# Kernel tuning notes

Measured on AMD Instinct MI355X. Metric: run time of the kernel, lower is better.

## Reference

```python
import jax, jax.numpy as jnp
import numpy as np

D_MODEL = 1024
NUM_HEADS = 16
D_FF = 4096
EPS = 1e-5


def setup_inputs() -> dict:
    key = jax.random.key(0)
    ks = jax.random.split(key, 8)
    B, S, D = 4, 2048, D_MODEL
    s = 1.0 / np.sqrt(D)
    return {
        "x": jax.random.normal(ks[0], (B, S, D), jnp.float32),
        "ln1_w": jnp.ones((D,), jnp.float32),
        "ln2_w": jnp.ones((D,), jnp.float32),
        "wq": jax.random.normal(ks[1], (D, D), jnp.float32) * s,
        "wk": jax.random.normal(ks[2], (D, D), jnp.float32) * s,
        "wv": jax.random.normal(ks[3], (D, D), jnp.float32) * s,
        "wo": jax.random.normal(ks[4], (D, D), jnp.float32) * s,
        "w1": jax.random.normal(ks[5], (D_FF, D), jnp.float32) * s,
        "w2": jax.random.normal(ks[6], (D, D_FF), jnp.float32) * (1.0 / np.sqrt(D_FF)),
    }


def rmsnorm(a, w):
    # (a * w) / sqrt(mean(a^2) + eps)  -- matches torch module exactly
    denom = jnp.sqrt(jnp.mean(jnp.square(a), axis=-1, keepdims=True) + EPS)
    return a * w / denom


def attention(x, wq, wk, wv, wo):
    B, S, D = x.shape
    H, dk = NUM_HEADS, D // NUM_HEADS
    q = (x @ wq.T).reshape(B, S, H, dk).transpose(0, 2, 1, 3)  # B H S dk
    k = (x @ wk.T).reshape(B, S, H, dk).transpose(0, 2, 1, 3)
    v = (x @ wv.T).reshape(B, S, H, dk).transpose(0, 2, 1, 3)
    scores = jnp.einsum("bhqd,bhkd->bhqk", q, k) / np.sqrt(dk)
    causal = jnp.triu(jnp.ones((S, S), bool), k=1)
    scores = jnp.where(causal, -jnp.inf, scores)
    probs = jax.nn.softmax(scores, axis=-1)
    out = jnp.einsum("bhqk,bhkd->bhqd", probs, v)
    out = out.transpose(0, 2, 1, 3).reshape(B, S, D)
    return out @ wo.T


def ffn(x, w1, w2):
    h = x @ w1.T
    h = 0.5 * h * (1.0 + jax.lax.erf(h / np.sqrt(2.0).astype(np.float32)))
    return h @ w2.T


def reference(x, ln1_w, ln2_w, wq, wk, wv, wo, w1, w2):
    y = x + attention(rmsnorm(x, ln1_w), wq, wk, wv, wo)
    return y + ffn(rmsnorm(y, ln2_w), w1, w2)
```

## Files before the change

### kernel.cpp

```cpp
#include <hip/hip_runtime.h>

#define DM    1024
#define DFF   4096
#define SEQ   2048
#define BATCH 4
#define NROWS (BATCH * SEQ)
#define HEADS 16
#define DKH   64
#define KSTR  (2 * DM)

typedef __attribute__((ext_vector_type(4))) float          f32x4;
typedef __attribute__((ext_vector_type(8))) __bf16         bf16x8;
typedef __attribute__((ext_vector_type(8))) unsigned short u16x8;
typedef __attribute__((ext_vector_type(4))) unsigned short u16x4;

static __device__ __forceinline__ unsigned short f2bf(float f) {
  unsigned u = __builtin_bit_cast(unsigned, f);
  u += 0x7fffu + ((u >> 16) & 1u);
  return (unsigned short)(u >> 16);
}

struct CvtJobs {
  const float* src[6];
  unsigned short* dst[6];
};
__constant__ const unsigned c_cum[6] = {262144u, 524288u, 786432u, 1048576u, 2097152u, 3145728u};

__global__ __launch_bounds__(256) void k_f2bf_all(CvtJobs jobs) {
  unsigned i = blockIdx.x * blockDim.x + threadIdx.x;
  if (i >= 3145728u) return;
  int j = 0;
#pragma unroll
  for (int s = 0; s < 6; ++s) j += (i >= c_cum[s]) ? 1 : 0;
  const unsigned base = (j == 0) ? 0u : c_cum[j - 1];
  const unsigned loc  = i - base;
  float4 v = reinterpret_cast<const float4*>(jobs.src[j])[loc];
  ushort4 o;
  o.x = f2bf(v.x); o.y = f2bf(v.y); o.z = f2bf(v.z); o.w = f2bf(v.w);
  reinterpret_cast<ushort4*>(jobs.dst[j])[loc] = o;
}

__global__ __launch_bounds__(256) void k_rmsnorm(const float* __restrict__ x,
                                                 const float* __restrict__ w,
                                                 unsigned short* __restrict__ out) {
  const int row = blockIdx.x;
  const float4 v = reinterpret_cast<const float4*>(x + (size_t)row * DM)[threadIdx.x];
  float ss = v.x * v.x + v.y * v.y + v.z * v.z + v.w * v.w;
#pragma unroll
  for (int off = 32; off > 0; off >>= 1) ss += __shfl_down(ss, off);
  __shared__ float red[4];
  if ((threadIdx.x & 63) == 0) red[threadIdx.x >> 6] = ss;
  __syncthreads();
  const float tot  = red[0] + red[1] + red[2] + red[3];
  const float rden = rsqrtf(tot * (1.0f / DM) + 1e-5f);
  const float4 wv = reinterpret_cast<const float4*>(w)[threadIdx.x];
  ushort4 o;
  o.x = f2bf(v.x * wv.x * rden);
  o.y = f2bf(v.y * wv.y * rden);
  o.z = f2bf(v.z * wv.z * rden);
  o.w = f2bf(v.w * wv.w * rden);
  reinterpret_cast<ushort4*>(out + (size_t)row * DM)[threadIdx.x] = o;
}

template <int EPI, int TN, int BK>
__global__ __launch_bounds__(256, 2) void k_gemm_nt(const unsigned short* __restrict__ A,
                                                    const unsigned short* __restrict__ B,
                                                    void* __restrict__ Cv,
                                                    const float* __restrict__ res,
                                                    int M, int N, int K) {
  constexpr int NW = TN / 128;
  alignas(16) __shared__ unsigned short As[2][128 * BK];
  alignas(16) __shared__ unsigned short Bs[2][128 * NW * BK];
  const int t  = threadIdx.x;
  const int w  = t >> 6;
  const int l  = t & 63;
  const int wr = w >> 1, wc = w & 1;
  const int lr = l & 15, lk = l >> 4;

  const unsigned bid = blockIdx.y * gridDim.x + blockIdx.x;
  const unsigned cpx = (gridDim.x * gridDim.y) >> 3;
  const unsigned sw  = (bid & 7) * cpx + (bid >> 3);
  const int m0 = (int)(sw / gridDim.x) * 128;
  const int n0 = (int)(sw % gridDim.x) * TN;

  auto stage = [&](int buf, int k0) {
    if constexpr (BK == 32) {
      const int srow = t >> 2;
      const int sgr  = (t & 3) ^ (srow & 3);
#pragma unroll
      for (int r = 0; r < 2; ++r) {
        const unsigned short* ga = A + (size_t)(m0 + r * 64 + srow) * K + k0 + 8 * sgr;
        __builtin_amdgcn_global_load_lds((__attribute__((address_space(1))) void*)ga,
                                         (__attribute__((address_space(3))) void*)(&As[buf][r * 2048 + w * 512]),
                                         16, 0, 0);
      }
#pragma unroll
      for (int r = 0; r < 2 * NW; ++r) {
        const unsigned short* gb = B + (size_t)(n0 + r * 64 + srow) * K + k0 + 8 * sgr;
        __builtin_amdgcn_global_load_lds((__attribute__((address_space(1))) void*)gb,
                                         (__attribute__((address_space(3))) void*)(&Bs[buf][r * 2048 + w * 512]),
                                         16, 0, 0);
      }
    } else {
      const int srow8 = l >> 3;
      const int g     = l & 7;
#pragma unroll
      for (int i = 0; i < 4; ++i) {
        const int row = i * 32 + w * 8 + srow8;
        const int sg  = g ^ (row & 7);
        const unsigned short* ga = A + (size_t)(m0 + row) * K + k0 + 8 * sg;
        __builtin_amdgcn_global_load_lds((__attribute__((address_space(1))) void*)ga,
                                         (__attribute__((address_space(3))) void*)(&As[buf][i * 2048 + w * 512]),
                                         16, 0, 0);
        const unsigned short* gb = B + (size_t)(n0 + row) * K + k0 + 8 * sg;
        __builtin_amdgcn_global_load_lds((__attribute__((address_space(1))) void*)gb,
                                         (__attribute__((address_space(3))) void*)(&Bs[buf][i * 2048 + w * 512]),
                                         16, 0, 0);
      }
    }
  };

  f32x4 acc[4][4 * NW] = {};

  stage(0, 0);
  const int nIt = K / BK;
  for (int it = 0; it < nIt; ++it) {
    const int buf = it & 1;
    __syncthreads();
    if (it + 1 < nIt) stage(buf ^ 1, (it + 1) * BK);

    if constexpr (BK == 32) {
      bf16x8 af[4], bf[4 * NW];
#pragma unroll
      for (int m = 0; m < 4; ++m)
        af[m] = *reinterpret_cast<const bf16x8*>(
            &As[buf][(wr * 64 + m * 16 + lr) * 32 + 8 * (lk ^ (lr & 3))]);
#pragma unroll
      for (int n = 0; n < 4 * NW; ++n)
        bf[n] = *reinterpret_cast<const bf16x8*>(
            &Bs[buf][(wc * 64 * NW + n * 16 + lr) * 32 + 8 * (lk ^ (lr & 3))]);
#pragma unroll
      for (int m = 0; m < 4; ++m)
#pragma unroll
        for (int n = 0; n < 4 * NW; ++n)
          acc[m][n] = __builtin_amdgcn_mfma_f32_16x16x32_bf16(af[m], bf[n], acc[m][n], 0, 0, 0);
    } else {
#pragma unroll
      for (int kk = 0; kk < 2; ++kk) {
        bf16x8 af[4], bf[4];
#pragma unroll
        for (int m = 0; m < 4; ++m)
          af[m] = *reinterpret_cast<const bf16x8*>(
              &As[buf][(wr * 64 + m * 16 + lr) * 64 + 8 * ((4 * kk + lk) ^ (lr & 7))]);
#pragma unroll
        for (int n = 0; n < 4; ++n)
          bf[n] = *reinterpret_cast<const bf16x8*>(
              &Bs[buf][(wc * 64 + n * 16 + lr) * 64 + 8 * ((4 * kk + lk) ^ (lr & 7))]);
#pragma unroll
        for (int m = 0; m < 4; ++m)
#pragma unroll
          for (int n = 0; n < 4; ++n)
            acc[m][n] = __builtin_amdgcn_mfma_f32_16x16x32_bf16(af[m], bf[n], acc[m][n], 0, 0, 0);
      }
    }
  }

#pragma unroll
  for (int m = 0; m < 4; ++m) {
#pragma unroll
    for (int n = 0; n < 4 * NW; ++n) {
#pragma unroll
      for (int r = 0; r < 4; ++r) {
        const size_t row = (size_t)(m0 + wr * 64 + m * 16 + lk * 4 + r);
        const size_t col = (size_t)(n0 + wc * 64 * NW + n * 16 + lr);
        const float a = acc[m][n][r];
        if constexpr (EPI == 0) {
          ((unsigned short*)Cv)[row * N + col] = f2bf(a);
        } else if constexpr (EPI == 1) {
          ((float*)Cv)[row * N + col] = a + res[row * N + col];
        } else if constexpr (EPI == 2) {
          const float h2 = a * a;
          const float e  = exp2f(a * (2.30221535f + 0.10295355f * h2));
          const float g  = a - a / (e + 1.0f);
          ((unsigned short*)Cv)[row * N + col] = f2bf(g);
        } else {
          const float sc = (col < DM) ? 0.18033688011f : 1.0f;
          ((unsigned short*)Cv)[row * N + col] = f2bf(a * sc);
        }
      }
    }
  }
}

__global__ __launch_bounds__(256, 3) void k_attn(const unsigned short* __restrict__ QK,
                                                 const unsigned short* __restrict__ VT,
                                                 unsigned short* __restrict__ O) {
  const int h   = blockIdx.x;
  const int qtA = blockIdx.y;
  const int qtB = 31 - qtA;
  const int b   = blockIdx.z;
  const int t  = threadIdx.x, w = t >> 6, l = t & 63;
  const int lr = l & 15, lk = l >> 4;
  const size_t rowB = (size_t)b * SEQ;
  const int hoff  = h * DKH;
  const int qw2[2] = { qtA * 64 + 16 * w, qtB * 64 + 16 * w };

  alignas(16) __shared__ unsigned short Ks[128 * 64];
  alignas(16) __shared__ unsigned short Vt[64 * 128];
  alignas(16) __shared__ unsigned short Ps[2][4][16 * 64];

  char* const KsB = (char*)Ks;
  char* const VtB = (char*)Vt;

  auto stage = [&](int kb2) {
#pragma unroll
    for (int i = 0; i < 4; ++i) {
      const int krow = 32 * w + 8 * i + (l >> 3);
      const int sgk  = (l & 7) ^ (krow & 7);
      const unsigned short* gk = QK + (size_t)(rowB + kb2 + krow) * KSTR + DM + hoff + 8 * sgk;
      __builtin_amdgcn_global_load_lds((__attribute__((address_space(1))) void*)gk,
                                       (__attribute__((address_space(3))) void*)(KsB + w * 4096 + i * 1024),
                                       16, 0, 0);
      const int vrow = 16 * w + 4 * i + (l >> 4);
      const int sgv  = (l & 15) ^ (vrow & 15);
      const unsigned short* gv = VT + (size_t)(hoff + vrow) * NROWS + rowB + kb2 + 8 * sgv;
      __builtin_amdgcn_global_load_lds((__attribute__((address_space(1))) void*)gv,
                                       (__attribute__((address_space(3))) void*)(VtB + w * 4096 + i * 1024),
                                       16, 0, 0);
    }
  };

  bf16x8 qf[2][2];
#pragma unroll
  for (int s = 0; s < 2; ++s)
#pragma unroll
    for (int kk = 0; kk < 2; ++kk)
      qf[s][kk] = *reinterpret_cast<const bf16x8*>(
          QK + (rowB + qw2[s] + lr) * KSTR + hoff + 32 * kk + 8 * lk);

  f32x4 oacc[2][4] = {};
  float mrun[2] = {-1e30f, -1e30f};
  float lrun[2] = {0.0f, 0.0f};

  const int ktmax = qtB >> 1;
  for (int kt = 0; kt <= ktmax; ++kt) {
    const int kbase = kt * 128;
    __syncthreads();
    stage(kbase);
    __syncthreads();

#pragma unroll
    for (int h2 = 0; h2 < 2; ++h2) {
      const int kb = kbase + 64 * h2;
      const bool act[2] = { kb <= qw2[0] + 15, kb <= qw2[1] + 15 };
      if (!act[0] && !act[1]) continue;
      const char* Kc = KsB + h2 * 8192;

      f32x4 sacc[2][4] = {};
      __builtin_amdgcn_s_setprio(1);
#pragma unroll
      for (int tt = 0; tt < 4; ++tt) {
        bf16x8 kf0 = *reinterpret_cast<const bf16x8*>(Kc + (16 * tt + lr) * 128 + 16 * ((lk + 0) ^ (lr & 7)));
        bf16x8 kf1 = *reinterpret_cast<const bf16x8*>(Kc + (16 * tt + lr) * 128 + 16 * ((lk + 4) ^ (lr & 7)));
#pragma unroll
        for (int s = 0; s < 2; ++s) {
          if (!act[s]) continue;
          sacc[s][tt] = __builtin_amdgcn_mfma_f32_16x16x32_bf16(kf0, qf[s][0], sacc[s][tt], 0, 0, 0);
          sacc[s][tt] = __builtin_amdgcn_mfma_f32_16x16x32_bf16(kf1, qf[s][1], sacc[s][tt], 0, 0, 0);
        }
      }
      __builtin_amdgcn_s_setprio(0);

#pragma unroll
      for (int s = 0; s < 2; ++s) {
        if (!act[s]) continue;
        const int qw = qw2[s];
        char* const PsSB = (char*)(Ps[s][w]);
        const int qg = qw + lr;
        float sv[4][4];
        if (kb + 63 > qw) {
#pragma unroll
          for (int tt = 0; tt < 4; ++tt)
#pragma unroll
            for (int r = 0; r < 4; ++r) {
              const int kg = kb + 16 * tt + 4 * lk + r;
              sv[tt][r] = (kg > qg) ? -1e30f : sacc[s][tt][r];
            }
        } else {
#pragma unroll
          for (int tt = 0; tt < 4; ++tt)
#pragma unroll
            for (int r = 0; r < 4; ++r) sv[tt][r] = sacc[s][tt][r];
        }
        const float a0 = fmaxf(fmaxf(sv[0][0], sv[0][1]), sv[0][2]);
        const float a1 = fmaxf(fmaxf(sv[0][3], sv[1][0]), sv[1][1]);
        const float a2 = fmaxf(fmaxf(sv[1][2], sv[1][3]), sv[2][0]);
        const float a3 = fmaxf(fmaxf(sv[2][1], sv[2][2]), sv[2][3]);
        const float a4 = fmaxf(fmaxf(sv[3][0], sv[3][1]), sv[3][2]);
        float tm = fmaxf(fmaxf(fmaxf(a0, a1), a2), fmaxf(fmaxf(a3, a4), sv[3][3]));
        tm = fmaxf(tm, __shfl_xor(tm, 16));
        tm = fmaxf(tm, __shfl_xor(tm, 32));
        float mref = mrun[s];
        if (__any(tm > mref + 8.0f)) {
          const float mnew  = fmaxf(mref, tm);
          const float alpha = exp2f(mref - mnew);
#pragma unroll
          for (int r = 0; r < 4; ++r) {
            const float ar = __shfl(alpha, 4 * lk + r);
#pragma unroll
            for (int dn = 0; dn < 4; ++dn) oacc[s][dn][r] *= ar;
          }
          lrun[s] *= alpha;
          mrun[s] = mnew;
          mref = mnew;
        }
        float p[4][4];
        unsigned short pb[4][4];
#pragma unroll
        for (int tt = 0; tt < 4; ++tt)
#pragma unroll
          for (int r = 0; r < 4; ++r) {
            p[tt][r] = exp2f(sv[tt][r] - mref);
            pb[tt][r] = __builtin_bit_cast(unsigned short, static_cast<__bf16>(p[tt][r]));
          }
        float t0 = (p[0][0] + p[0][1]) + (p[0][2] + p[0][3]);
        float t1 = (p[1][0] + p[1][1]) + (p[1][2] + p[1][3]);
        float t2 = (p[2][0] + p[2][1]) + (p[2][2] + p[2][3]);
        float t3 = (p[3][0] + p[3][1]) + (p[3][2] + p[3][3]);
        float ts = (t0 + t1) + (t2 + t3);
        ts += __shfl_xor(ts, 16);
        ts += __shfl_xor(ts, 32);
        lrun[s] += ts;
#pragma unroll
        for (int tt = 0; tt < 4; ++tt) {
          u16x4 pw = {pb[tt][0], pb[tt][1], pb[tt][2], pb[tt][3]};
          *reinterpret_cast<u16x4*>(
              PsSB + lr * 128 + ((32 * tt + 8 * lk) ^ (16 * (lr & 7)))) = pw;
        }
      }

      asm volatile("" ::: "memory");

#pragma unroll
      for (int kk = 0; kk < 2; ++kk) {
        bf16x8 vf[4];
#pragma unroll
        for (int dn = 0; dn < 4; ++dn)
          vf[dn] = *reinterpret_cast<const bf16x8*>(
              VtB + (16 * dn + lr) * 256 + 16 * ((8 * h2 + 4 * kk + lk) ^ lr));
        __builtin_amdgcn_s_setprio(1);
#pragma unroll
        for (int s = 0; s < 2; ++s) {
          if (!act[s]) continue;
          char* const PsSB = (char*)(Ps[s][w]);
          bf16x8 pa = *reinterpret_cast<const bf16x8*>(
              PsSB + lr * 128 + ((64 * kk + 16 * lk) ^ (16 * (lr & 7))));
#pragma unroll
          for (int dn = 0; dn < 4; ++dn)
            oacc[s][dn] = __builtin_amdgcn_mfma_f32_16x16x32_bf16(pa, vf[dn], oacc[s][dn], 0, 0, 0);
        }
        __builtin_amdgcn_s_setprio(0);
      }

      asm volatile("" ::: "memory");
    }
  }

#pragma unroll
  for (int s = 0; s < 2; ++s)
#pragma unroll
    for (int r = 0; r < 4; ++r) {
      const float li = 1.0f / __shfl(lrun[s], 4 * lk + r);
      const size_t row = rowB + qw2[s] + 4 * lk + r;
#pragma unroll
      for (int dn = 0; dn < 4; ++dn)
        O[row * DM + hoff + 16 * dn + lr] = f2bf(oacc[s][dn][r] * li);
    }
}

extern "C" void kernel_launch(void* const* d_in, const int* in_sizes, int n_in,
                              void* d_out, int out_size, void* d_ws, size_t ws_size,
                              hipStream_t stream) {
  const float* x   = (const float*)d_in[0];
  const float* ln1 = (const float*)d_in[1];
  const float* ln2 = (const float*)d_in[2];
  const float* wq  = (const float*)d_in[3];
  const float* wk  = (const float*)d_in[4];
  const float* wv  = (const float*)d_in[5];
  const float* wo  = (const float*)d_in[6];
  const float* w1  = (const float*)d_in[7];
  const float* w2  = (const float*)d_in[8];

  char* ws = (char*)d_ws;
  size_t off = 0;
  auto take = [&](size_t bytes) { void* p = ws + off; off += bytes; return p; };
  unsigned short* wqkb = (unsigned short*)take((size_t)2 * DM * DM * 2);
  unsigned short* wvb  = (unsigned short*)take((size_t)DM * DM * 2);
  unsigned short* wob  = (unsigned short*)take((size_t)DM * DM * 2);
  unsigned short* w1b  = (unsigned short*)take((size_t)DFF * DM * 2);
  unsigned short* w2b  = (unsigned short*)take((size_t)DM * DFF * 2);
  unsigned short* qk   = (unsigned short*)take((size_t)NROWS * 2 * DM * 2);
  unsigned short* xn   = (unsigned short*)take((size_t)NROWS * DM * 2);
  unsigned short* vtb  = (unsigned short*)take((size_t)DM * NROWS * 2);
  float*          yb   = (float*)take((size_t)NROWS * DM * 4);
  unsigned short* hb   = (unsigned short*)take((size_t)NROWS * DFF * 2);
  unsigned short* yn   = qk;

  CvtJobs jobs;
  jobs.src[0] = wq;  jobs.dst[0] = wqkb;
  jobs.src[1] = wk;  jobs.dst[1] = wqkb + (size_t)DM * DM;
  jobs.src[2] = wv;  jobs.dst[2] = wvb;
  jobs.src[3] = wo;  jobs.dst[3] = wob;
  jobs.src[4] = w1;  jobs.dst[4] = w1b;
  jobs.src[5] = w2;  jobs.dst[5] = w2b;
  k_f2bf_all<<<dim3(3145728u / 256u), dim3(256), 0, stream>>>(jobs);

  k_rmsnorm<<<dim3(NROWS), dim3(256), 0, stream>>>(x, ln1, xn);

  k_gemm_nt<3, 256, 32><<<dim3(2 * DM / 256, NROWS / 128), dim3(256), 0, stream>>>(
      xn, wqkb, qk, nullptr, NROWS, 2 * DM, DM);

  k_gemm_nt<0, 128, 64><<<dim3(NROWS / 128, DM / 128), dim3(256), 0, stream>>>(
      wvb, xn, vtb, nullptr, DM, NROWS, DM);

  k_attn<<<dim3(HEADS, 16, BATCH), dim3(256), 0, stream>>>(qk, vtb, xn);

  k_gemm_nt<1, 128, 64><<<dim3(DM / 128, NROWS / 128), dim3(256), 0, stream>>>(
      xn, wob, yb, x, NROWS, DM, DM);

  k_rmsnorm<<<dim3(NROWS), dim3(256), 0, stream>>>(yb, ln2, yn);

  k_gemm_nt<2, 256, 32><<<dim3(DFF / 256, NROWS / 128), dim3(256), 0, stream>>>(
      yn, w1b, hb, nullptr, NROWS, DFF, DM);
  k_gemm_nt<1, 128, 64><<<dim3(DM / 128, NROWS / 128), dim3(256), 0, stream>>>(
      hb, w2b, (float*)d_out, yb, NROWS, DM, DFF);
}
```

Measured before the change: 377.8 us.

## Merge weight conversion with RMSNorm and fuse QK and V^T GEMMs into one launch

The weight bf16 conversion and the first RMSNorm now run in a single launch, with block ranges dispatched to each job. The QK projection (previously 128x256 tiles, BK=32) and the V-transpose GEMM are merged into one kernel that uses a shared 128x128x64 body with direct global-to-LDS loads and XOR swizzling. The goal is to cut launch gaps and tail underutilisation between small kernels. The trade-offs are a changed tile shape for the QK GEMM and a branch on block index that splits grid work unevenly.

```diff
diff --git a/kernel.cpp b/kernel.cpp
--- a/kernel.cpp
+++ b/kernel.cpp
@@ -25,19 +25,42 @@
   unsigned short* dst[6];
 };
 __constant__ const unsigned c_cum[6] = {262144u, 524288u, 786432u, 1048576u, 2097152u, 3145728u};
-
-__global__ __launch_bounds__(256) void k_f2bf_all(CvtJobs jobs) {
-  unsigned i = blockIdx.x * blockDim.x + threadIdx.x;
-  if (i >= 3145728u) return;
-  int j = 0;
-#pragma unroll
-  for (int s = 0; s < 6; ++s) j += (i >= c_cum[s]) ? 1 : 0;
-  const unsigned base = (j == 0) ? 0u : c_cum[j - 1];
-  const unsigned loc  = i - base;
-  float4 v = reinterpret_cast<const float4*>(jobs.src[j])[loc];
-  ushort4 o;
-  o.x = f2bf(v.x); o.y = f2bf(v.y); o.z = f2bf(v.z); o.w = f2bf(v.w);
-  reinterpret_cast<ushort4*>(jobs.dst[j])[loc] = o;
+#define CVT_BLOCKS 12288u
+
+__global__ __launch_bounds__(256) void k_pre(CvtJobs jobs,
+                                             const float* __restrict__ x,
+                                             const float* __restrict__ ln1,
+                                             unsigned short* __restrict__ xn) {
+  if (blockIdx.x < CVT_BLOCKS) {
+    const unsigned i = blockIdx.x * 256u + threadIdx.x;
+    int j = 0;
+#pragma unroll
+    for (int s = 0; s < 6; ++s) j += (i >= c_cum[s]) ? 1 : 0;
+    const unsigned base = (j == 0) ? 0u : c_cum[j - 1];
+    const unsigned loc  = i - base;
+    float4 v = reinterpret_cast<const float4*>(jobs.src[j])[loc];
+    ushort4 o;
+    o.x = f2bf(v.x); o.y = f2bf(v.y); o.z = f2bf(v.z); o.w = f2bf(v.w);
+    reinterpret_cast<ushort4*>(jobs.dst[j])[loc] = o;
+  } else {
+    const int row = (int)(blockIdx.x - CVT_BLOCKS);
+    const float4 v = reinterpret_cast<const float4*>(x + (size_t)row * DM)[threadIdx.x];
+    float ss = v.x * v.x + v.y * v.y + v.z * v.z + v.w * v.w;
+#pragma unroll
+    for (int off = 32; off > 0; off >>= 1) ss += __shfl_down(ss, off);
+    __shared__ float red[4];
+    if ((threadIdx.x & 63) == 0) red[threadIdx.x >> 6] = ss;
+    __syncthreads();
+    const float tot  = red[0] + red[1] + red[2] + red[3];
+    const float rden = rsqrtf(tot * (1.0f / DM) + 1e-5f);
+    const float4 wv = reinterpret_cast<const float4*>(ln1)[threadIdx.x];
+    ushort4 o;
+    o.x = f2bf(v.x * wv.x * rden);
+    o.y = f2bf(v.y * wv.y * rden);
+    o.z = f2bf(v.z * wv.z * rden);
+    o.w = f2bf(v.w * wv.w * rden);
+    reinterpret_cast<ushort4*>(xn + (size_t)row * DM)[threadIdx.x] = o;
+  }
 }
 
 __global__ __launch_bounds__(256) void k_rmsnorm(const float* __restrict__ x,
@@ -60,6 +83,100 @@
   o.z = f2bf(v.z * wv.z * rden);
   o.w = f2bf(v.w * wv.w * rden);
   reinterpret_cast<ushort4*>(out + (size_t)row * DM)[threadIdx.x] = o;
+}
+
+__device__ __forceinline__ void gemm_body_128_64(const unsigned short* __restrict__ A,
+                                                 const unsigned short* __restrict__ B,
+                                                 unsigned short* __restrict__ C,
+                                                 int M, int N, int K, bool prescale,
+                                                 unsigned vbid, unsigned vgx, unsigned vgy,
+                                                 unsigned short* AsP, unsigned short* BsP) {
+  const int t  = threadIdx.x;
+  const int w  = t >> 6;
+  const int l  = t & 63;
+  const int wr = w >> 1, wc = w & 1;
+  const int lr = l & 15, lk = l >> 4;
+
+  const unsigned cpx = (vgx * vgy) >> 3;
+  const unsigned sw  = (vbid & 7) * cpx + (vbid >> 3);
+  const int m0 = (int)(sw / vgx) * 128;
+  const int n0 = (int)(sw % vgx) * 128;
+
+  const int srow8 = l >> 3;
+  const int g     = l & 7;
+
+  auto stage = [&](int buf, int k0) {
+#pragma unroll
+    for (int i = 0; i < 4; ++i) {
+      const int row = i * 32 + w * 8 + srow8;
+      const int sg  = g ^ (row & 7);
+      const unsigned short* ga = A + (size_t)(m0 + row) * K + k0 + 8 * sg;
+      __builtin_amdgcn_global_load_lds((__attribute__((address_space(1))) void*)ga,
+                                       (__attribute__((address_space(3))) void*)(AsP + buf * 8192 + i * 2048 + w * 512),
+                                       16, 0, 0);
+      const unsigned short* gb = B + (size_t)(n0 + row) * K + k0 + 8 * sg;
+      __builtin_amdgcn_global_load_lds((__attribute__((address_space(1))) void*)gb,
+                                       (__attribute__((address_space(3))) void*)(BsP + buf * 8192 + i * 2048 + w * 512),
+                                       16, 0, 0);
+    }
+  };
+
+  f32x4 acc[4][4] = {};
+
+  stage(0, 0);
+  const int nIt = K >> 6;
+  for (int it = 0; it < nIt; ++it) {
+    const int buf = it & 1;
+    __syncthreads();
+    if (it + 1 < nIt) stage(buf ^ 1, (it + 1) << 6);
+
+#pragma unroll
+    for (int kk = 0; kk < 2; ++kk) {
+      bf16x8 af[4], bf[4];
+#pragma unroll
+      for (int m = 0; m < 4; ++m)
+        af[m] = *reinterpret_cast<const bf16x8*>(
+            AsP + buf * 8192 + (wr * 64 + m * 16 + lr) * 64 + 8 * ((4 * kk + lk) ^ (lr & 7)));
+#pragma unroll
+      for (int n = 0; n < 4; ++n)
+        bf[n] = *reinterpret_cast<const bf16x8*>(
+            BsP + buf * 8192 + (wc * 64 + n * 16 + lr) * 64 + 8 * ((4 * kk + lk) ^ (lr & 7)));
+#pragma unroll
+      for (int m = 0; m < 4; ++m)
+#pragma unroll
+        for (int n = 0; n < 4; ++n)
+          acc[m][n] = __builtin_amdgcn_mfma_f32_16x16x32_bf16(af[m], bf[n], acc[m][n], 0, 0, 0);
+    }
+  }
+
+#pragma unroll
+  for (int m = 0; m < 4; ++m) {
+#pragma unroll
+    for (int n = 0; n < 4; ++n) {
+#pragma unroll
+      for (int r = 0; r < 4; ++r) {
+        const size_t row = (size_t)(m0 + wr * 64 + m * 16 + lk * 4 + r);
+        const size_t col = (size_t)(n0 + wc * 64 + n * 16 + lr);
+        const float sc = (prescale && col < DM) ? 0.18033688011f : 1.0f;
+        C[row * N + col] = f2bf(acc[m][n][r] * sc);
+      }
+    }
+  }
+}
+
+__global__ __launch_bounds__(256, 2) void k_qkvt(const unsigned short* __restrict__ xn,
+                                                 const unsigned short* __restrict__ wqkb,
+                                                 unsigned short* __restrict__ qk,
+                                                 const unsigned short* __restrict__ wvb,
+                                                 unsigned short* __restrict__ vtb) {
+  alignas(16) __shared__ unsigned short As[2][128 * 64];
+  alignas(16) __shared__ unsigned short Bs[2][128 * 64];
+  const unsigned bid = blockIdx.x;
+  if (bid < 1024u) {
+    gemm_body_128_64(xn, wqkb, qk, NROWS, 2 * DM, DM, true, bid, 16, 64, &As[0][0], &Bs[0][0]);
+  } else {
+    gemm_body_128_64(wvb, xn, vtb, DM, NROWS, DM, false, bid - 1024u, 64, 8, &As[0][0], &Bs[0][0]);
+  }
 }
 
 template <int EPI, int TN, int BK>
@@ -174,18 +291,13 @@
         const size_t row = (size_t)(m0 + wr * 64 + m * 16 + lk * 4 + r);
         const size_t col = (size_t)(n0 + wc * 64 * NW + n * 16 + lr);
         const float a = acc[m][n][r];
-        if constexpr (EPI == 0) {
-          ((unsigned short*)Cv)[row * N + col] = f2bf(a);
-        } else if constexpr (EPI == 1) {
+        if constexpr (EPI == 1) {
           ((float*)Cv)[row * N + col] = a + res[row * N + col];
-        } else if constexpr (EPI == 2) {
+        } else {
           const float h2 = a * a;
           const float e  = exp2f(a * (2.30221535f + 0.10295355f * h2));
           const float g  = a - a / (e + 1.0f);
           ((unsigned short*)Cv)[row * N + col] = f2bf(g);
-        } else {
-          const float sc = (col < DM) ? 0.18033688011f : 1.0f;
-          ((unsigned short*)Cv)[row * N + col] = f2bf(a * sc);
         }
       }
     }
@@ -413,15 +525,10 @@
   jobs.src[3] = wo;  jobs.dst[3] = wob;
   jobs.src[4] = w1;  jobs.dst[4] = w1b;
   jobs.src[5] = w2;  jobs.dst[5] = w2b;
-  k_f2bf_all<<<dim3(3145728u / 256u), dim3(256), 0, stream>>>(jobs);
-
-  k_rmsnorm<<<dim3(NROWS), dim3(256), 0, stream>>>(x, ln1, xn);
-
-  k_gemm_nt<3, 256, 32><<<dim3(2 * DM / 256, NROWS / 128), dim3(256), 0, stream>>>(
-      xn, wqkb, qk, nullptr, NROWS, 2 * DM, DM);
-
-  k_gemm_nt<0, 128, 64><<<dim3(NROWS / 128, DM / 128), dim3(256), 0, stream>>>(
-      wvb, xn, vtb, nullptr, DM, NROWS, DM);
+
+  k_pre<<<dim3(CVT_BLOCKS + NROWS), dim3(256), 0, stream>>>(jobs, x, ln1, xn);
+
+  k_qkvt<<<dim3(1536), dim3(256), 0, stream>>>(xn, wqkb, qk, wvb, vtb);
 
   k_attn<<<dim3(HEADS, 16, BATCH), dim3(256), 0, stream>>>(qk, vtb, xn);
 
```

Result: no change. 373.3 us (-1.2%).
